# Optimization experiments

Hardware: AMD Instinct MI355X
Metric: run time of the kernel (lower is better)

Reference implementation:

```python
import jax, jax.numpy as jnp
import numpy as np

EMB_DIM = 4096
INNER = 1024
VOCAB = 32000
NPRED = 3
B, N = 2, 512
EPS = 1e-6
# weighting constants from MLPSpeculator.__init__
STATE_W = 0.5 ** (0.5 / NPRED)
ALPHA = float(np.sqrt((1.0 - STATE_W ** 2) * (INNER / 2.0)) / STATE_W)  # emb_weight / state_weight


def _ln(x, w, b):
    # LayerNormParameterized with use_mean=False (fms default): RMS-style norm + scale + shift
    x = x * jax.lax.rsqrt(jnp.mean(x * x, axis=-1, keepdims=True) + EPS)
    return x * w + b


def setup_inputs() -> dict:
    key = jax.random.key(0)
    ks = jax.random.split(key, 8)
    s = 1.0 / np.sqrt(INNER)  # reset_parameters init scale
    return {
        "state": jax.random.normal(ks[0], (B, N, EMB_DIM), jnp.float32),
        "inds": jax.random.randint(ks[1], (B, N + NPRED), 0, VOCAB, dtype=jnp.int32),
        "emb_w": jax.random.normal(ks[2], (NPRED, VOCAB, INNER), jnp.float32) * s,
        "proj0_w": jax.random.normal(ks[3], (INNER, EMB_DIM), jnp.float32) * s,
        "proj_w": jax.random.normal(ks[4], (NPRED - 1, INNER, INNER), jnp.float32) * s,
        "head_w": jax.random.normal(ks[5], (NPRED, VOCAB, INNER), jnp.float32) * s,
        "ln_w": jnp.ones((NPRED, INNER), jnp.float32),
        "ln_b": jnp.zeros((NPRED, INNER), jnp.float32),
    }


def reference(state, inds, emb_w, proj0_w, proj_w, head_w, ln_w, ln_b):
    n = state.shape[1]
    outs = []
    for i in range(NPRED):
        z = emb_w[i][inds[:, i:i + n]]                      # [b, n, inner] gather
        W = proj0_w if i == 0 else proj_w[i - 1]            # [inner, emb_dim] or [inner, inner]
        state = jnp.einsum('bnd,id->bni', state, W)
        state = state + ALPHA * z                           # torch.add(..., alpha=emb_w/state_w)
        state = jax.nn.gelu(_ln(state, ln_w[i], ln_b[i]), approximate=False)
        outs.append(jnp.einsum('bni,vi->bnv', state, head_w[i]))  # logits [b, n, vocab]
    return jnp.stack(outs, axis=0)                          # [n_predict, b, n, vocab]
```

## Files before the change

### kernel.cpp

```cpp
#include <hip/hip_runtime.h>
#include <hip/hip_bf16.h>
#include <math.h>

#define EMB_DIM 4096
#define INNER   1024
#define VOCAB   32000
#define NPRED   3
#define SEQ     512
#define TOKENS  1024

typedef __attribute__((ext_vector_type(8))) short bf16x8;
typedef __attribute__((ext_vector_type(4))) float f32x4;

__device__ inline void gload_lds16(const void* g, void* l) {
  __builtin_amdgcn_global_load_lds(
      (const __attribute__((address_space(1))) void*)g,
      (__attribute__((address_space(3))) void*)l, 16, 0, 0);
}

__device__ inline unsigned short f2bf(float f) {
  unsigned u = __float_as_uint(f);
  u += 0x7fffu + ((u >> 16) & 1u);
  return (unsigned short)(u >> 16);
}

__global__ void cvt_kernel(const float4* __restrict__ in, ushort4* __restrict__ out, int n4) {
  int stride = gridDim.x * blockDim.x;
  for (int i = blockIdx.x * blockDim.x + threadIdx.x; i < n4; i += stride) {
    float4 v = in[i];
    ushort4 o;
    o.x = f2bf(v.x); o.y = f2bf(v.y); o.z = f2bf(v.z); o.w = f2bf(v.w);
    out[i] = o;
  }
}

__global__ __launch_bounds__(256) void proj_cvt(const __hip_bfloat16* __restrict__ A,
                                                const __hip_bfloat16* __restrict__ Bw,
                                                float* __restrict__ C, int K,
                                                const float4* __restrict__ cvsrc,
                                                ushort4* __restrict__ cvdst, int n4) {
  if (blockIdx.x >= 64) {
    for (int i = (blockIdx.x - 64) * 256 + threadIdx.x; i < n4; i += 960 * 256) {
      float4 v = cvsrc[i];
      ushort4 o;
      o.x = f2bf(v.x); o.y = f2bf(v.y); o.z = f2bf(v.z); o.w = f2bf(v.w);
      cvdst[i] = o;
    }
    return;
  }
  __shared__ char smem[16384];
  char* As = smem;
  char* Bs = smem + 8192;

  const int tid  = threadIdx.x;
  const int lane = tid & 63;
  const int wave = tid >> 6;
  const int wm = wave >> 1, wn = wave & 1;

  const int bm = (blockIdx.x >> 3) * 128;
  const int bn = (blockIdx.x & 7) * 128;
  const int N = 1024;

  const char* Ag = (const char*)(A  + (size_t)(bm + (tid >> 2)) * K + (tid & 3) * 8);
  const char* Bg = (const char*)(Bw + (size_t)(bn + (tid >> 2)) * K + (tid & 3) * 8);
  const size_t rowskip = (size_t)64 * K * 2;

  f32x4 acc[4][4] = {};

  const int fa = (wm * 64 + (lane & 15)) * 64 + (lane >> 4) * 16;
  const int fb = (wn * 64 + (lane & 15)) * 64 + (lane >> 4) * 16;

  for (int k0 = 0; k0 < K; k0 += 32) {
    gload_lds16(Ag,           As + tid * 16);
    gload_lds16(Ag + rowskip, As + 4096 + tid * 16);
    gload_lds16(Bg,           Bs + tid * 16);
    gload_lds16(Bg + rowskip, Bs + 4096 + tid * 16);
    Ag += 64; Bg += 64;
    __syncthreads();

    bf16x8 af[4], bfv[4];
#pragma unroll
    for (int m = 0; m < 4; ++m) af[m]  = *(const bf16x8*)(As + fa + m * 1024);
#pragma unroll
    for (int n = 0; n < 4; ++n) bfv[n] = *(const bf16x8*)(Bs + fb + n * 1024);
#pragma unroll
    for (int m = 0; m < 4; ++m)
#pragma unroll
      for (int n = 0; n < 4; ++n)
        acc[m][n] = __builtin_amdgcn_mfma_f32_16x16x32_bf16(af[m], bfv[n], acc[m][n], 0, 0, 0);
    __syncthreads();
  }

  const int r0 = bm + wm * 64 + (lane >> 4) * 4;
  const int c0 = bn + wn * 64 + (lane & 15);
#pragma unroll
  for (int m = 0; m < 4; ++m)
#pragma unroll
    for (int n = 0; n < 4; ++n) {
      float* Cp = C + (size_t)(r0 + m * 16) * N + (c0 + n * 16);
#pragma unroll
      for (int r = 0; r < 4; ++r)
        Cp[(size_t)r * N] = acc[m][n][r];
    }
}

__global__ __launch_bounds__(512, 2) void gemm256(const __hip_bfloat16* __restrict__ A,
                                                  const __hip_bfloat16* __restrict__ B,
                                                  float* __restrict__ C,
                                                  int M, int N, int K) {
  __shared__ char smem[131072];
  const int tid  = threadIdx.x;
  const int lane = tid & 63;
  const int wave = tid >> 6;
  const int wm = wave >> 2;
  const int wn = wave & 3;

  const int MT = M >> 8;
  const int nwg = gridDim.x;
  const int o = blockIdx.x;
  const int q = nwg >> 3, r = nwg & 7;
  const int xcd = o & 7, idx = o >> 3;
  const int wg = (xcd < r ? xcd * (q + 1) : r * (q + 1) + (xcd - r) * q) + idx;
  const int bm = (wg % MT) * 256;
  const int bn = (wg / MT) * 256;

  f32x4 acc[8][4] = {};

  const int sl   = (lane >> 4) ^ ((lane >> 1) & 3);
  const int aoff = (wm * 128 + (lane & 15)) * 64 + sl * 16;
  const int boff = (wn * 64  + (lane & 15)) * 64 + sl * 16;

#define STAGE_T(PTR, BASEROW, LDSBASE, KT_)                                     \
  {                                                                             \
    _Pragma("unroll")                                                           \
    for (int c = 0; c < 2; ++c) {                                               \
      int chunk = c * 512 + tid;                                                \
      int row = chunk >> 2;                                                     \
      int s = (chunk & 3) ^ ((row >> 1) & 3);                                   \
      gload_lds16(PTR + (size_t)((BASEROW) + row) * K + (KT_) * 32 + s * 8,     \
                  smem + (LDSBASE) + chunk * 16);                               \
    }                                                                           \
  }

  STAGE_T(A, bm, 0,             0)
  STAGE_T(B, bn, 65536,         0)
  STAGE_T(A, bm, 16384,         1)
  STAGE_T(B, bn, 65536 + 16384, 1)
  STAGE_T(A, bm, 32768,         2)
  STAGE_T(B, bn, 65536 + 32768, 2)

  const int KT = K >> 5;
  for (int t = 0; t < KT; ++t) {
    const int bc = (t & 3) * 16384;
    const int bs = ((t + 3) & 3) * 16384;
    const char* Ab = smem + bc;
    const char* Bb = smem + 65536 + bc;

    asm volatile("s_waitcnt vmcnt(8)" ::: "memory");
    __builtin_amdgcn_s_barrier();

    const int pk = (t + 3 < KT) ? t + 3 : KT - 1;

    bf16x8 af0[4], bfv[4];
#pragma unroll
    for (int m = 0; m < 4; ++m) af0[m] = *(const bf16x8*)(Ab + aoff + m * 1024);
#pragma unroll
    for (int n = 0; n < 4; ++n) bfv[n] = *(const bf16x8*)(Bb + boff + n * 1024);
    STAGE_T(A, bm, bs, pk)
    asm volatile("s_waitcnt lgkmcnt(0)" ::: "memory");
    __builtin_amdgcn_sched_barrier(0);
    __builtin_amdgcn_s_setprio(1);
#pragma unroll
    for (int m = 0; m < 4; ++m)
#pragma unroll
      for (int n = 0; n < 4; ++n)
        acc[m][n] = __builtin_amdgcn_mfma_f32_16x16x32_bf16(af0[m], bfv[n], acc[m][n], 0, 0, 0);
    __builtin_amdgcn_s_setprio(0);

    bf16x8 af1[4];
#pragma unroll
    for (int m = 0; m < 4; ++m) af1[m] = *(const bf16x8*)(Ab + aoff + (m + 4) * 1024);
    STAGE_T(B, bn, 65536 + bs, pk)
    asm volatile("s_waitcnt lgkmcnt(0)" ::: "memory");
    __builtin_amdgcn_sched_barrier(0);
    __builtin_amdgcn_s_setprio(1);
#pragma unroll
    for (int m = 0; m < 4; ++m)
#pragma unroll
      for (int n = 0; n < 4; ++n)
        acc[m + 4][n] = __builtin_amdgcn_mfma_f32_16x16x32_bf16(af1[m], bfv[n], acc[m + 4][n], 0, 0, 0);
    __builtin_amdgcn_s_setprio(0);
    __builtin_amdgcn_sched_barrier(0);
  }
  asm volatile("s_waitcnt vmcnt(0)" ::: "memory");

  const int r0 = bm + wm * 128 + (lane >> 4) * 4;
  const int c0 = bn + wn * 64 + (lane & 15);
#pragma unroll
  for (int m = 0; m < 8; ++m)
#pragma unroll
    for (int n = 0; n < 4; ++n) {
      float* Cp = C + (size_t)(r0 + m * 16) * N + (c0 + n * 16);
#pragma unroll
      for (int rr = 0; rr < 4; ++rr)
        Cp[(size_t)rr * N] = acc[m][n][rr];
    }
#undef STAGE_T
}

__global__ __launch_bounds__(256) void fuse_ln_gelu(const float* __restrict__ ns,
    const float* __restrict__ emb,
    const int* __restrict__ inds,
    const float* __restrict__ lnw, const float* __restrict__ lnb,
    ushort4* __restrict__ out_bf16,
    int i, float alpha)
{
  const int t = blockIdx.x;
  const int b = t >> 9, n = t & 511;
  const int idx = inds[b * (SEQ + NPRED) + n + i];

  const float4* x = (const float4*)(ns + (size_t)t * INNER);
  const float4* z = (const float4*)(emb + (size_t)idx * INNER);
  const int j = threadIdx.x;

  float4 xv = x[j], zv = z[j];
  float4 v;
  v.x = xv.x + alpha * zv.x;
  v.y = xv.y + alpha * zv.y;
  v.z = xv.z + alpha * zv.z;
  v.w = xv.w + alpha * zv.w;

  float ss = v.x * v.x + v.y * v.y + v.z * v.z + v.w * v.w;
#pragma unroll
  for (int o = 32; o > 0; o >>= 1) ss += __shfl_down(ss, o);
  __shared__ float red[4];
  if ((threadIdx.x & 63) == 0) red[threadIdx.x >> 6] = ss;
  __syncthreads();
  float total = red[0] + red[1] + red[2] + red[3];
  float r = rsqrtf(total * (1.0f / INNER) + 1e-6f);

  float4 wv = ((const float4*)lnw)[j];
  float4 bv = ((const float4*)lnb)[j];
  const float inv_sqrt2 = 0.70710678118654752f;
  ushort4 o;
  float y;
  y = v.x * r * wv.x + bv.x; o.x = f2bf(0.5f * y * (1.0f + erff(y * inv_sqrt2)));
  y = v.y * r * wv.y + bv.y; o.y = f2bf(0.5f * y * (1.0f + erff(y * inv_sqrt2)));
  y = v.z * r * wv.z + bv.z; o.z = f2bf(0.5f * y * (1.0f + erff(y * inv_sqrt2)));
  y = v.w * r * wv.w + bv.w; o.w = f2bf(0.5f * y * (1.0f + erff(y * inv_sqrt2)));

  out_bf16[(size_t)t * (INNER / 4) + j] = o;
}

extern "C" void kernel_launch(void* const* d_in, const int* in_sizes, int n_in,
                              void* d_out, int out_size, void* d_ws, size_t ws_size,
                              hipStream_t stream) {
  const float* state = (const float*)d_in[0];
  const int*   inds  = (const int*)d_in[1];
  const float* emb_w = (const float*)d_in[2];
  const float* proj0 = (const float*)d_in[3];
  const float* projw = (const float*)d_in[4];
  const float* headw = (const float*)d_in[5];
  const float* lnw   = (const float*)d_in[6];
  const float* lnb   = (const float*)d_in[7];
  float* out = (float*)d_out;

  char* ws = (char*)d_ws;
  __hip_bfloat16* stateA = (__hip_bfloat16*)(ws);
  __hip_bfloat16* stateI = (__hip_bfloat16*)(ws + 8388608);
  float*          nsf    = (float*)        (ws + 10485760);
  __hip_bfloat16* p0b    = (__hip_bfloat16*)(ws + 14680064);
  __hip_bfloat16* pwb    = (__hip_bfloat16*)(ws + 23068672);
  __hip_bfloat16* hb     = (__hip_bfloat16*)(ws + 27262976);

  double sw = pow(0.5, 1.0 / 6.0);
  float alpha = (float)(sqrt((1.0 - sw * sw) * (INNER / 2.0)) / sw);

  auto cvt = [&](const float* src, __hip_bfloat16* dst, size_t n) {
    int n4 = (int)(n / 4);
    int blocks = (n4 + 255) / 256;
    if (blocks > 2048) blocks = 2048;
    cvt_kernel<<<dim3(blocks), dim3(256), 0, stream>>>((const float4*)src, (ushort4*)dst, n4);
  };

  cvt(state, stateA, (size_t)TOKENS * EMB_DIM);
  cvt(proj0, p0b, (size_t)INNER * EMB_DIM);
  cvt(projw, pwb, (size_t)2 * INNER * INNER);

  for (int i = 0; i < NPRED; ++i) {
    const __hip_bfloat16* Ab = (i == 0) ? stateA : stateI;
    const __hip_bfloat16* Bb = (i == 0) ? p0b : pwb + (size_t)(i - 1) * INNER * INNER;
    int K = (i == 0) ? EMB_DIM : INNER;

    proj_cvt<<<dim3(1024), dim3(256), 0, stream>>>(Ab, Bb, nsf, K,
        (const float4*)(headw + (size_t)i * VOCAB * INNER), (ushort4*)hb,
        (int)((size_t)VOCAB * INNER / 4));

    fuse_ln_gelu<<<dim3(TOKENS), dim3(256), 0, stream>>>(nsf,
        emb_w + (size_t)i * VOCAB * INNER, inds,
        lnw + i * INNER, lnb + i * INNER, (ushort4*)stateI, i, alpha);

    gemm256<<<dim3(500), dim3(512), 0, stream>>>(stateI, hb,
        out + (size_t)i * TOKENS * VOCAB, TOKENS, VOCAB, INNER);
  }
}
```

Baseline: 439.1 us.

## Restructure head GEMM into double-buffered 64-wide K steps with four barrier-separated phases

The head GEMM moves from a 4-deep ring of 32-wide K slices to two 64 KB buffers, each holding a 64-wide K tile (two 32-wide halves). Each loop iteration now runs four MFMA phases with s_barrier between them, issuing global-to-LDS loads for the next tile while computing the current one. The aim is to cut the number of outer iterations and interleave memory traffic more evenly with compute, in the style of an 8-phase schedule. In exchange it adds many more workgroup barriers per iteration, and prefetch depth drops from three slices ahead to one tile ahead.

Result: no change. 445.8 us (+1.5%).

```diff
diff --git a/kernel.cpp b/kernel.cpp
--- a/kernel.cpp
+++ b/kernel.cpp
@@ -104,10 +104,10 @@
     }
 }
 
-__global__ __launch_bounds__(512, 2) void gemm256(const __hip_bfloat16* __restrict__ A,
-                                                  const __hip_bfloat16* __restrict__ B,
-                                                  float* __restrict__ C,
-                                                  int M, int N, int K) {
+__global__ __launch_bounds__(512, 2) void gemm256_8p(const __hip_bfloat16* __restrict__ A,
+                                                     const __hip_bfloat16* __restrict__ B,
+                                                     float* __restrict__ C,
+                                                     int M, int N, int K) {
   __shared__ char smem[131072];
   const int tid  = threadIdx.x;
   const int lane = tid & 63;
@@ -130,43 +130,38 @@
   const int aoff = (wm * 128 + (lane & 15)) * 64 + sl * 16;
   const int boff = (wn * 64  + (lane & 15)) * 64 + sl * 16;
 
-#define STAGE_T(PTR, BASEROW, LDSBASE, KT_)                                     \
+#define STAGE_U(PTR, BASEROW, LDSBASE, T_, KQ_)                                 \
   {                                                                             \
     _Pragma("unroll")                                                           \
     for (int c = 0; c < 2; ++c) {                                               \
       int chunk = c * 512 + tid;                                                \
       int row = chunk >> 2;                                                     \
       int s = (chunk & 3) ^ ((row >> 1) & 3);                                   \
-      gload_lds16(PTR + (size_t)((BASEROW) + row) * K + (KT_) * 32 + s * 8,     \
+      gload_lds16(PTR + (size_t)((BASEROW) + row) * K + (T_) * 64 + (KQ_) * 32 + s * 8, \
                   smem + (LDSBASE) + chunk * 16);                               \
     }                                                                           \
   }
 
-  STAGE_T(A, bm, 0,             0)
-  STAGE_T(B, bn, 65536,         0)
-  STAGE_T(A, bm, 16384,         1)
-  STAGE_T(B, bn, 65536 + 16384, 1)
-  STAGE_T(A, bm, 32768,         2)
-  STAGE_T(B, bn, 65536 + 32768, 2)
-
-  const int KT = K >> 5;
+  STAGE_U(A, bm, 0,             0, 0)
+  STAGE_U(B, bn, 32768,         0, 0)
+  STAGE_U(A, bm, 16384,         0, 1)
+  STAGE_U(B, bn, 49152,         0, 1)
+  asm volatile("s_waitcnt vmcnt(4)" ::: "memory");
+  __builtin_amdgcn_s_barrier();
+
+  const int KT = K >> 6;
   for (int t = 0; t < KT; ++t) {
-    const int bc = (t & 3) * 16384;
-    const int bs = ((t + 3) & 3) * 16384;
-    const char* Ab = smem + bc;
-    const char* Bb = smem + 65536 + bc;
-
-    asm volatile("s_waitcnt vmcnt(8)" ::: "memory");
-    __builtin_amdgcn_s_barrier();
-
-    const int pk = (t + 3 < KT) ? t + 3 : KT - 1;
-
-    bf16x8 af0[4], bfv[4];
-#pragma unroll
-    for (int m = 0; m < 4; ++m) af0[m] = *(const bf16x8*)(Ab + aoff + m * 1024);
-#pragma unroll
-    for (int n = 0; n < 4; ++n) bfv[n] = *(const bf16x8*)(Bb + boff + n * 1024);
-    STAGE_T(A, bm, bs, pk)
+    const int lp = (t & 1) << 16;
+    const int lo = ((t + 1) & 1) << 16;
+    const int pt = (t + 1 < KT) ? t + 1 : KT - 1;
+    bf16x8 af[4], bfv[4];
+
+#pragma unroll
+    for (int m = 0; m < 4; ++m) af[m]  = *(const bf16x8*)(smem + lp + aoff + m * 1024);
+#pragma unroll
+    for (int n = 0; n < 4; ++n) bfv[n] = *(const bf16x8*)(smem + lp + 32768 + boff + n * 1024);
+    STAGE_U(A, bm, lo, pt, 0)
+    __builtin_amdgcn_s_barrier();
     asm volatile("s_waitcnt lgkmcnt(0)" ::: "memory");
     __builtin_amdgcn_sched_barrier(0);
     __builtin_amdgcn_s_setprio(1);
@@ -174,13 +169,15 @@
     for (int m = 0; m < 4; ++m)
 #pragma unroll
       for (int n = 0; n < 4; ++n)
-        acc[m][n] = __builtin_amdgcn_mfma_f32_16x16x32_bf16(af0[m], bfv[n], acc[m][n], 0, 0, 0);
+        acc[m][n] = __builtin_amdgcn_mfma_f32_16x16x32_bf16(af[m], bfv[n], acc[m][n], 0, 0, 0);
     __builtin_amdgcn_s_setprio(0);
-
-    bf16x8 af1[4];
-#pragma unroll
-    for (int m = 0; m < 4; ++m) af1[m] = *(const bf16x8*)(Ab + aoff + (m + 4) * 1024);
-    STAGE_T(B, bn, 65536 + bs, pk)
+    __builtin_amdgcn_s_barrier();
+
+#pragma unroll
+    for (int m = 0; m < 4; ++m) af[m] = *(const bf16x8*)(smem + lp + 4096 + aoff + m * 1024);
+    STAGE_U(B, bn, lo + 32768, pt, 0)
+    asm volatile("s_waitcnt vmcnt(4)" ::: "memory");
+    __builtin_amdgcn_s_barrier();
     asm volatile("s_waitcnt lgkmcnt(0)" ::: "memory");
     __builtin_amdgcn_sched_barrier(0);
     __builtin_amdgcn_s_setprio(1);
@@ -188,9 +185,42 @@
     for (int m = 0; m < 4; ++m)
 #pragma unroll
       for (int n = 0; n < 4; ++n)
-        acc[m + 4][n] = __builtin_amdgcn_mfma_f32_16x16x32_bf16(af1[m], bfv[n], acc[m + 4][n], 0, 0, 0);
+        acc[m + 4][n] = __builtin_amdgcn_mfma_f32_16x16x32_bf16(af[m], bfv[n], acc[m + 4][n], 0, 0, 0);
     __builtin_amdgcn_s_setprio(0);
+    __builtin_amdgcn_s_barrier();
+
+#pragma unroll
+    for (int m = 0; m < 4; ++m) af[m]  = *(const bf16x8*)(smem + lp + 16384 + aoff + m * 1024);
+#pragma unroll
+    for (int n = 0; n < 4; ++n) bfv[n] = *(const bf16x8*)(smem + lp + 49152 + boff + n * 1024);
+    STAGE_U(A, bm, lo + 16384, pt, 1)
+    __builtin_amdgcn_s_barrier();
+    asm volatile("s_waitcnt lgkmcnt(0)" ::: "memory");
     __builtin_amdgcn_sched_barrier(0);
+    __builtin_amdgcn_s_setprio(1);
+#pragma unroll
+    for (int m = 0; m < 4; ++m)
+#pragma unroll
+      for (int n = 0; n < 4; ++n)
+        acc[m][n] = __builtin_amdgcn_mfma_f32_16x16x32_bf16(af[m], bfv[n], acc[m][n], 0, 0, 0);
+    __builtin_amdgcn_s_setprio(0);
+    __builtin_amdgcn_s_barrier();
+
+#pragma unroll
+    for (int m = 0; m < 4; ++m) af[m] = *(const bf16x8*)(smem + lp + 16384 + 4096 + aoff + m * 1024);
+    STAGE_U(B, bn, lo + 49152, pt, 1)
+    asm volatile("s_waitcnt vmcnt(4)" ::: "memory");
+    __builtin_amdgcn_s_barrier();
+    asm volatile("s_waitcnt lgkmcnt(0)" ::: "memory");
+    __builtin_amdgcn_sched_barrier(0);
+    __builtin_amdgcn_s_setprio(1);
+#pragma unroll
+    for (int m = 0; m < 4; ++m)
+#pragma unroll
+      for (int n = 0; n < 4; ++n)
+        acc[m + 4][n] = __builtin_amdgcn_mfma_f32_16x16x32_bf16(af[m], bfv[n], acc[m + 4][n], 0, 0, 0);
+    __builtin_amdgcn_s_setprio(0);
+    __builtin_amdgcn_s_barrier();
   }
   asm volatile("s_waitcnt vmcnt(0)" ::: "memory");
 
@@ -205,7 +235,7 @@
       for (int rr = 0; rr < 4; ++rr)
         Cp[(size_t)rr * N] = acc[m][n][rr];
     }
-#undef STAGE_T
+#undef STAGE_U
 }
 
 __global__ __launch_bounds__(256) void fuse_ln_gelu(const float* __restrict__ ns,
@@ -300,7 +330,7 @@
         emb_w + (size_t)i * VOCAB * INNER, inds,
         lnw + i * INNER, lnb + i * INNER, (ushort4*)stateI, i, alpha);
 
-    gemm256<<<dim3(500), dim3(512), 0, stream>>>(stateI, hb,
+    gemm256_8p<<<dim3(500), dim3(512), 0, stream>>>(stateI, hb,
         out + (size_t)i * TOKENS * VOCAB, TOKENS, VOCAB, INNER);
   }
 }
```

## Merge head GEMM, next projection GEMM and next head-weight conversion into one launch

Applied to the files above, without the earlier changes.

Replaces the per-step sequence of projection+convert, LN/GELU and head GEMM with a single 'mega' kernel whose blocks are split by role. Blocks 0-499 run the vocab head GEMM for step i, blocks 500-563 compute the next step's small projection GEMM into nsf, and the remaining blocks convert the next head weight to bf16 into a double-buffered slot. This overlaps the bandwidth-bound weight conversion and the small GEMM with the compute-bound head GEMM and removes launches, at the cost of sharing CUs and memory bandwidth among the roles. The roles are independent within a launch: the projection reads stateI, which the head GEMM also reads, and nsf and stateI are not overwritten until the following fuse launch.

Measured after the change: 441.5 us. No clear change (+0.6%).

```diff
diff --git a/kernel.cpp b/kernel.cpp
--- a/kernel.cpp
+++ b/kernel.cpp
@@ -104,21 +104,81 @@
     }
 }
 
-__global__ __launch_bounds__(512, 2) void gemm256(const __hip_bfloat16* __restrict__ A,
-                                                  const __hip_bfloat16* __restrict__ B,
-                                                  float* __restrict__ C,
-                                                  int M, int N, int K) {
+__global__ __launch_bounds__(512, 2) void mega(const __hip_bfloat16* __restrict__ A,
+                                               const __hip_bfloat16* __restrict__ B,
+                                               float* __restrict__ C,
+                                               const __hip_bfloat16* __restrict__ Pw,
+                                               float* __restrict__ nsf,
+                                               const float4* __restrict__ cvsrc,
+                                               ushort4* __restrict__ cvdst, int n4) {
   __shared__ char smem[131072];
   const int tid  = threadIdx.x;
   const int lane = tid & 63;
   const int wave = tid >> 6;
+
+  if (blockIdx.x >= 564) {
+    for (int i = (blockIdx.x - 564) * 512 + tid; i < n4; i += 460 * 512) {
+      float4 v = cvsrc[i];
+      ushort4 o;
+      o.x = f2bf(v.x); o.y = f2bf(v.y); o.z = f2bf(v.z); o.w = f2bf(v.w);
+      cvdst[i] = o;
+    }
+    return;
+  }
+
+  if (blockIdx.x >= 500) {
+    char* As = smem;
+    char* Bs = smem + 8192;
+    const int p = blockIdx.x - 500;
+    const int bm = (p >> 3) * 128;
+    const int bn = (p & 7) * 128;
+    const int wm = wave >> 2, wn = wave & 3;
+
+    const char* Ag = (const char*)(A  + (size_t)(bm + (tid >> 2)) * INNER + (tid & 3) * 8);
+    const char* Bg = (const char*)(Pw + (size_t)(bn + (tid >> 2)) * INNER + (tid & 3) * 8);
+
+    f32x4 acc[4][2] = {};
+    const int fa = (wm * 64 + (lane & 15)) * 64 + (lane >> 4) * 16;
+    const int fb = (wn * 32 + (lane & 15)) * 64 + (lane >> 4) * 16;
+
+    for (int k0 = 0; k0 < INNER; k0 += 32) {
+      gload_lds16(Ag, As + tid * 16);
+      gload_lds16(Bg, Bs + tid * 16);
+      Ag += 64; Bg += 64;
+      __syncthreads();
+      bf16x8 af[4], bfv[2];
+#pragma unroll
+      for (int m = 0; m < 4; ++m) af[m]  = *(const bf16x8*)(As + fa + m * 1024);
+#pragma unroll
+      for (int n = 0; n < 2; ++n) bfv[n] = *(const bf16x8*)(Bs + fb + n * 1024);
+#pragma unroll
+      for (int m = 0; m < 4; ++m)
+#pragma unroll
+        for (int n = 0; n < 2; ++n)
+          acc[m][n] = __builtin_amdgcn_mfma_f32_16x16x32_bf16(af[m], bfv[n], acc[m][n], 0, 0, 0);
+      __syncthreads();
+    }
+    const int r0 = bm + wm * 64 + (lane >> 4) * 4;
+    const int c0 = bn + wn * 32 + (lane & 15);
+#pragma unroll
+    for (int m = 0; m < 4; ++m)
+#pragma unroll
+      for (int n = 0; n < 2; ++n) {
+        float* Cp = nsf + (size_t)(r0 + m * 16) * INNER + (c0 + n * 16);
+#pragma unroll
+        for (int r = 0; r < 4; ++r)
+          Cp[(size_t)r * INNER] = acc[m][n][r];
+      }
+    return;
+  }
+
+  const int M = TOKENS, N = VOCAB, K = INNER;
   const int wm = wave >> 2;
   const int wn = wave & 3;
 
   const int MT = M >> 8;
-  const int nwg = gridDim.x;
   const int o = blockIdx.x;
-  const int q = nwg >> 3, r = nwg & 7;
+  const int q = 500 >> 3, r = 500 & 7;
   const int xcd = o & 7, idx = o >> 3;
   const int wg = (xcd < r ? xcd * (q + 1) : r * (q + 1) + (xcd - r) * q) + idx;
   const int bm = (wg % MT) * 256;
@@ -271,7 +331,8 @@
   float*          nsf    = (float*)        (ws + 10485760);
   __hip_bfloat16* p0b    = (__hip_bfloat16*)(ws + 14680064);
   __hip_bfloat16* pwb    = (__hip_bfloat16*)(ws + 23068672);
-  __hip_bfloat16* hb     = (__hip_bfloat16*)(ws + 27262976);
+  __hip_bfloat16* hb0    = (__hip_bfloat16*)(ws + 27262976);
+  __hip_bfloat16* hb1    = (__hip_bfloat16*)(ws + 92798976);
 
   double sw = pow(0.5, 1.0 / 6.0);
   float alpha = (float)(sqrt((1.0 - sw * sw) * (INNER / 2.0)) / sw);
@@ -283,24 +344,31 @@
     cvt_kernel<<<dim3(blocks), dim3(256), 0, stream>>>((const float4*)src, (ushort4*)dst, n4);
   };
 
+  const int hn4 = (int)((size_t)VOCAB * INNER / 4);
+
   cvt(state, stateA, (size_t)TOKENS * EMB_DIM);
   cvt(proj0, p0b, (size_t)INNER * EMB_DIM);
   cvt(projw, pwb, (size_t)2 * INNER * INNER);
 
-  for (int i = 0; i < NPRED; ++i) {
-    const __hip_bfloat16* Ab = (i == 0) ? stateA : stateI;
-    const __hip_bfloat16* Bb = (i == 0) ? p0b : pwb + (size_t)(i - 1) * INNER * INNER;
-    int K = (i == 0) ? EMB_DIM : INNER;
-
-    proj_cvt<<<dim3(1024), dim3(256), 0, stream>>>(Ab, Bb, nsf, K,
-        (const float4*)(headw + (size_t)i * VOCAB * INNER), (ushort4*)hb,
-        (int)((size_t)VOCAB * INNER / 4));
-
-    fuse_ln_gelu<<<dim3(TOKENS), dim3(256), 0, stream>>>(nsf,
-        emb_w + (size_t)i * VOCAB * INNER, inds,
-        lnw + i * INNER, lnb + i * INNER, (ushort4*)stateI, i, alpha);
-
-    gemm256<<<dim3(500), dim3(512), 0, stream>>>(stateI, hb,
-        out + (size_t)i * TOKENS * VOCAB, TOKENS, VOCAB, INNER);
-  }
-}
+  proj_cvt<<<dim3(1024), dim3(256), 0, stream>>>(stateA, p0b, nsf, EMB_DIM,
+      (const float4*)headw, (ushort4*)hb0, hn4);
+  fuse_ln_gelu<<<dim3(TOKENS), dim3(256), 0, stream>>>(nsf,
+      emb_w, inds, lnw, lnb, (ushort4*)stateI, 0, alpha);
+
+  mega<<<dim3(1024), dim3(512), 0, stream>>>(stateI, hb0, out,
+      pwb, nsf,
+      (const float4*)(headw + (size_t)1 * VOCAB * INNER), (ushort4*)hb1, hn4);
+  fuse_ln_gelu<<<dim3(TOKENS), dim3(256), 0, stream>>>(nsf,
+      emb_w + (size_t)1 * VOCAB * INNER, inds,
+      lnw + INNER, lnb + INNER, (ushort4*)stateI, 1, alpha);
+
+  mega<<<dim3(1024), dim3(512), 0, stream>>>(stateI, hb1, out + (size_t)TOKENS * VOCAB,
+      pwb + (size_t)INNER * INNER, nsf,
+      (const float4*)(headw + (size_t)2 * VOCAB * INNER), (ushort4*)hb0, hn4);
+  fuse_ln_gelu<<<dim3(TOKENS), dim3(256), 0, stream>>>(nsf,
+      emb_w + (size_t)2 * VOCAB * INNER, inds,
+      lnw + 2 * INNER, lnb + 2 * INNER, (ushort4*)stateI, 2, alpha);
+
+  mega<<<dim3(500), dim3(512), 0, stream>>>(stateI, hb0, out + (size_t)2 * TOKENS * VOCAB,
+      pwb, nsf, (const float4*)headw, (ushort4*)hb1, hn4);
+}
```
